# Performance work log

Hardware: AMD Instinct MI355X
Metric: run time of the kernel (lower is better)

Reference implementation:

```python
import jax, jax.numpy as jnp
import numpy as np

N_NODES = 22
K_NEIGHBOR = 4
BN_EPS = 1e-5


def _conv1d(x, w):
    # x: (B, C, L), w: (O, C, 7), stride 1, padding 3
    return jax.lax.conv_general_dilated(x, w, (1,), [(3, 3)],
                                        dimension_numbers=('NCH', 'OIH', 'NCH'))


def _block(x, w, gamma, beta):
    # x: (N, B, C, L) -> conv + per-node BatchNorm (train-mode batch stats,
    # matching the original per-node loop) + ReLU + MaxPool1d(2)
    n, b, c, l = x.shape
    y = _conv1d(x.reshape(n * b, c, l), w)            # (N*B, O, L)
    o, lo = y.shape[1], y.shape[2]
    y = y.reshape(n, b, o, lo)
    mean = y.mean(axis=(1, 3), keepdims=True)
    var = y.var(axis=(1, 3), keepdims=True)
    y = (y - mean) * jax.lax.rsqrt(var + BN_EPS)
    y = y * gamma[None, None, :, None] + beta[None, None, :, None]
    y = jax.nn.relu(y)
    y = y.reshape(n, b, o, lo // 2, 2).max(axis=-1)   # MaxPool1d(2)
    return y


def _adj_matrix(feat, k):
    # feat: (B, N, D). Squared euclidean distances, k nearest (incl. self), row-normalized.
    sq = jnp.sum(feat ** 2, axis=2, keepdims=True)            # (B, N, 1)
    dist = sq + jnp.swapaxes(sq, 1, 2) - 2.0 * jnp.einsum('bnd,bmd->bnm', feat, feat)
    _, idx = jax.lax.top_k(-dist, k)                          # smallest-k indices, (B, N, k)
    adj = jax.nn.one_hot(idx, feat.shape[1], dtype=feat.dtype).sum(axis=2)
    return adj * (1.0 / k)


def setup_inputs() -> dict:
    key = jax.random.key(0)
    ks = jax.random.split(key, 20)
    B, N, T = 256, N_NODES, 2000
    f32 = jnp.float32
    inp = {
        'x': jax.random.normal(ks[0], (B, N, T), f32),
        # conv stack (shared across all electrode nodes)
        'w1': jax.random.normal(ks[1], (4, 1, 7), f32) * 0.2,
        'g1': jnp.ones((4,), f32), 'b1': jnp.zeros((4,), f32),
        'w2': jax.random.normal(ks[2], (8, 4, 7), f32) * 0.1,
        'g2': jnp.ones((8,), f32), 'b2': jnp.zeros((8,), f32),
        'w3': jax.random.normal(ks[3], (16, 8, 7), f32) * 0.1,
        'g3': jnp.ones((16,), f32), 'b3': jnp.zeros((16,), f32),
        # graph convolutions (uniform init like torch module)
        'gw1': jax.random.uniform(ks[4], (16, 32), f32, -1/np.sqrt(32), 1/np.sqrt(32)),
        'gb1': jax.random.uniform(ks[5], (1, 1, 32), f32, -1/np.sqrt(32), 1/np.sqrt(32)),
        'gw2': jax.random.uniform(ks[6], (32, 64), f32, -1/np.sqrt(64), 1/np.sqrt(64)),
        'gb2': jax.random.uniform(ks[7], (1, 1, 64), f32, -1/np.sqrt(64), 1/np.sqrt(64)),
        'gw3': jax.random.uniform(ks[8], (64, 128), f32, -1/np.sqrt(128), 1/np.sqrt(128)),
        'gb3': jax.random.uniform(ks[9], (1, 1, 128), f32, -1/np.sqrt(128), 1/np.sqrt(128)),
        # heads (stored as (in, out))
        'fw1': jax.random.normal(ks[10], (128, 64), f32) * 0.05,
        'fb1': jnp.zeros((64,), f32),
        'fw2': jax.random.normal(ks[11], (64, 4), f32) * 0.05,
        'fb2': jnp.zeros((4,), f32),
    }
    return inp


def reference(x, w1, g1, b1, w2, g2, b2, w3, g3, b3,
              gw1, gb1, gw2, gb2, gw3, gb3, fw1, fb1, fw2, fb2):
    B, N, T = x.shape
    # --- MultiChannelConv (vectorized over electrode nodes) ---
    h = jnp.transpose(x, (1, 0, 2))[:, :, None, :]   # (N, B, 1, T)
    h = _block(h, w1, g1, b1)                        # (N, B, 4, T/2)
    h = _block(h, w2, g2, b2)                        # (N, B, 8, T/4)
    h = _block(h, w3, g3, b3)                        # (N, B, 16, T/8)
    feat = h.mean(axis=-1)                           # AdaptiveAvgPool1d(1) -> (N, B, 16)
    feat = jnp.transpose(feat, (1, 0, 2))            # (B, N, 16)
    # --- adjacency from top-k nearest neighbors ---
    adj = _adj_matrix(feat, K_NEIGHBOR)              # (B, N, N)
    # --- graph convolutions ---
    x1 = jax.nn.relu(jnp.einsum('bnm,bmf->bnf', adj, feat @ gw1) + gb1)
    x2 = jax.nn.relu(jnp.einsum('bnm,bmf->bnf', adj, x1 @ gw2) + gb2)
    x3 = jax.nn.relu(jnp.einsum('bnm,bmf->bnf', adj, x2 @ gw3) + gb3)
    # mean over nodes, then MLP head
    pooled = x3.mean(axis=1)                         # (B, 128)
    out = (pooled @ fw1 + fb1) @ fw2 + fb2           # (B, nclass)
    return out
```

## Files before the change

kernel.cpp:

```cpp
#include <hip/hip_runtime.h>

#define BSZ 256
#define NND 22
#define BN_EPS 1e-5f

template<int CIN, int COUT, int R, int SROW>
__device__ __forceinline__ void conv_coreR(
    const float (*s_in)[SROW], const float* s_w, int tid, float y[COUT][R]) {
#pragma unroll
  for (int o = 0; o < COUT; o++)
#pragma unroll
    for (int r = 0; r < R; r++) y[o][r] = 0.f;
#pragma unroll 1
  for (int c = 0; c < CIN; c++) {
    float xr[R + 6];
    if constexpr (R == 4) {
      const float4* xp = (const float4*)&s_in[c][4 * tid];
      float4 xa = xp[0], xb = xp[1];
      float2 xc = *(const float2*)&s_in[c][4 * tid + 8];
      xr[0] = xa.x; xr[1] = xa.y; xr[2] = xa.z; xr[3] = xa.w;
      xr[4] = xb.x; xr[5] = xb.y; xr[6] = xb.z; xr[7] = xb.w;
      xr[8] = xc.x; xr[9] = xc.y;
    } else {
      const float2* xp = (const float2*)&s_in[c][2 * tid];
      float2 x0 = xp[0], x1 = xp[1], x2 = xp[2], x3 = xp[3];
      xr[0] = x0.x; xr[1] = x0.y; xr[2] = x1.x; xr[3] = x1.y;
      xr[4] = x2.x; xr[5] = x2.y; xr[6] = x3.x; xr[7] = x3.y;
    }
#pragma unroll
    for (int k = 0; k < 7; k++) {
      const float4* wp = (const float4*)&s_w[(c * 7 + k) * COUT];
#pragma unroll
      for (int o4 = 0; o4 < COUT / 4; o4++) {
        float4 wv = wp[o4];
#pragma unroll
        for (int r = 0; r < R; r++) {
          y[4 * o4 + 0][r] += wv.x * xr[r + k];
          y[4 * o4 + 1][r] += wv.y * xr[r + k];
          y[4 * o4 + 2][r] += wv.z * xr[r + k];
          y[4 * o4 + 3][r] += wv.w * xr[r + k];
        }
      }
    }
  }
}

template<int CIN, int COUT, int NTH>
__device__ __forceinline__ void stage_weights(const float* __restrict__ w,
                                              float* s_w, int tid) {
  for (int i = tid; i < CIN * 7 * COUT; i += NTH) {
    int c = i / (7 * COUT), k = (i / COUT) % 7, o = i % COUT;
    s_w[i] = w[(o * CIN + c) * 7 + k];
  }
}

__global__ __launch_bounds__(256) void prep_weights(
    const float* __restrict__ w2, const float* __restrict__ w3,
    float* __restrict__ w2t, float* __restrict__ w3t) {
  int tid = threadIdx.x;
  if (tid < 224) {
    int c = tid / 56, k = (tid / 8) % 7, o = tid & 7;
    w2t[tid] = w2[(o * 4 + c) * 7 + k];
  }
  for (int i = tid; i < 896; i += 256) {
    int c = i / 112, k = (i / 16) % 7, o = i & 15;
    w3t[i] = w3[(o * 8 + c) * 7 + k];
  }
}

template<int CIN, int COUT, int LIN, int NTH, int NT, int R>
__global__ __launch_bounds__(NTH) void conv_statsR(
    const float* __restrict__ in, long sn, long sb, long sc,
    const float* __restrict__ w, float* __restrict__ part) {
  const int TILE = R * NTH;
  const int SROW = TILE + 8;
  __shared__ alignas(16) float s_in[CIN][SROW];
  __shared__ alignas(16) float s_w[CIN * 7 * COUT];
  __shared__ float s_red[2][NTH / 64][COUT];
  int tid = threadIdx.x, n = blockIdx.z, b = blockIdx.y;
  int t0 = blockIdx.x * TILE;
  const float* base = in + (long)n * sn + (long)b * sb;
  stage_weights<CIN, COUT, NTH>(w, s_w, tid);
  for (int c = 0; c < CIN; c++)
    for (int i = tid; i < TILE + 6; i += NTH) {
      int l = t0 + i - 3;
      s_in[c][i] = (l >= 0 && l < LIN) ? base[(long)c * sc + l] : 0.f;
    }
  __syncthreads();
  float y[COUT][R];
  conv_coreR<CIN, COUT, R, SROW>(s_in, s_w, tid, y);
  bool valid = (t0 + R * tid) < LIN;
  int lane = tid & 63, wv = tid >> 6;
#pragma unroll
  for (int o = 0; o < COUT; o++) {
    float s = 0.f, q = 0.f;
    if (valid) {
#pragma unroll
      for (int r = 0; r < R; r++) { s += y[o][r]; q += y[o][r] * y[o][r]; }
    }
#pragma unroll
    for (int off = 32; off > 0; off >>= 1) {
      s += __shfl_down(s, off, 64);
      q += __shfl_down(q, off, 64);
    }
    if (lane == 0) { s_red[0][wv][o] = s; s_red[1][wv][o] = q; }
  }
  __syncthreads();
  if (tid < COUT) {
    float s = 0.f, q = 0.f;
#pragma unroll
    for (int g = 0; g < NTH / 64; g++) { s += s_red[0][g][tid]; q += s_red[1][g][tid]; }
    long slot = ((long)n * NT + blockIdx.x) * BSZ + b;
    part[slot * (2 * COUT) + tid] = s;
    part[slot * (2 * COUT) + COUT + tid] = q;
  }
}

template<int C, int NSLOT, int LIN>
__global__ __launch_bounds__(256) void stats_reduce(
    const float* __restrict__ part,
    const float* __restrict__ gamma, const float* __restrict__ beta,
    float* __restrict__ scs) {
  const int V = 2 * C;
  const int GRP = 256 / V;
  int n = blockIdx.x, tid = threadIdx.x;
  int j = tid % V, g = tid / V;
  const float* p = part + (long)n * NSLOT * V;
  float s = 0.f;
  for (int sl = g; sl < NSLOT; sl += GRP) s += p[(long)sl * V + j];
  __shared__ float red[V][GRP];
  __shared__ float tot[V];
  red[j][g] = s;
  __syncthreads();
  if (tid < V) {
    float t = 0.f;
#pragma unroll
    for (int gg = 0; gg < GRP; gg++) t += red[tid][gg];
    tot[tid] = t;
  }
  __syncthreads();
  if (tid < C) {
    float cnt = (float)BSZ * (float)LIN;
    float m = tot[tid] / cnt;
    float var = tot[C + tid] / cnt - m * m;
    float istd = 1.0f / sqrtf(var + BN_EPS);
    float scl = gamma[tid] * istd;
    scs[n * 64 + tid] = scl;
    scs[n * 64 + 32 + tid] = beta[tid] - m * scl;
  }
}

__global__ __launch_bounds__(256) void fused1(
    const float* __restrict__ x,
    const float* __restrict__ w1,
    const float* __restrict__ scs1,
    const float* __restrict__ w2t,
    float* __restrict__ y2p,
    float* __restrict__ p2) {
  __shared__ alignas(16) float s_x[2016];
  __shared__ alignas(16) float s_h1[4][1008];
  __shared__ float s_sc[4], s_sh[4];
  __shared__ float s_red[2][4][8];
  int tid = threadIdx.x, n = blockIdx.z, b = blockIdx.y;
  const float* xb = x + (long)b * (NND * 2000) + (long)n * 2000;
  if (tid < 4) { s_sc[tid] = scs1[n * 64 + tid]; s_sh[tid] = scs1[n * 64 + 32 + tid]; }
  for (int i = tid; i < 500; i += 256)
    *(float4*)&s_x[4 * i + 4] = *(const float4*)&xb[4 * i];
  if (tid == 0) {
    *(float4*)&s_x[0] = make_float4(0.f, 0.f, 0.f, 0.f);
    *(float4*)&s_x[2004] = make_float4(0.f, 0.f, 0.f, 0.f);
  }
  __syncthreads();
  if (tid < 250) {
    float xr[16];
    const float4* xp = (const float4*)&s_x[8 * tid];
#pragma unroll
    for (int v = 0; v < 4; v++) {
      float4 t = xp[v];
      xr[4 * v + 0] = t.x; xr[4 * v + 1] = t.y;
      xr[4 * v + 2] = t.z; xr[4 * v + 3] = t.w;
    }
    float y[4][8];
#pragma unroll
    for (int o = 0; o < 4; o++)
#pragma unroll
      for (int r = 0; r < 8; r++) y[o][r] = 0.f;
#pragma unroll
    for (int k = 0; k < 7; k++) {
      float w0 = w1[0 * 7 + k], w1v = w1[1 * 7 + k];
      float w2v = w1[2 * 7 + k], w3v = w1[3 * 7 + k];
#pragma unroll
      for (int r = 0; r < 8; r++) {
        y[0][r] += w0 * xr[r + k + 1];
        y[1][r] += w1v * xr[r + k + 1];
        y[2][r] += w2v * xr[r + k + 1];
        y[3][r] += w3v * xr[r + k + 1];
      }
    }
#pragma unroll
    for (int o = 0; o < 4; o++) {
      float a0 = y[o][0] * s_sc[o] + s_sh[o], a1 = y[o][1] * s_sc[o] + s_sh[o];
      float a2 = y[o][2] * s_sc[o] + s_sh[o], a3 = y[o][3] * s_sc[o] + s_sh[o];
      float a4 = y[o][4] * s_sc[o] + s_sh[o], a5 = y[o][5] * s_sc[o] + s_sh[o];
      float a6 = y[o][6] * s_sc[o] + s_sh[o], a7 = y[o][7] * s_sc[o] + s_sh[o];
      float4 v;
      v.x = fmaxf(fmaxf(a0, a1), 0.f);
      v.y = fmaxf(fmaxf(a2, a3), 0.f);
      v.z = fmaxf(fmaxf(a4, a5), 0.f);
      v.w = fmaxf(fmaxf(a6, a7), 0.f);
      *(float4*)&s_h1[o][4 * tid + 4] = v;
    }
  }
  if (tid < 4) {
    *(float4*)&s_h1[tid][0] = make_float4(0.f, 0.f, 0.f, 0.f);
    *(float4*)&s_h1[tid][1004] = make_float4(0.f, 0.f, 0.f, 0.f);
  }
  __syncthreads();
  float y2[8][4];
#pragma unroll
  for (int o = 0; o < 8; o++)
#pragma unroll
    for (int r = 0; r < 4; r++) y2[o][r] = 0.f;
  if (tid < 250) {
#pragma unroll 1
    for (int c = 0; c < 4; c++) {
      float xr[12];
      const float4* xp = (const float4*)&s_h1[c][4 * tid];
#pragma unroll
      for (int v = 0; v < 3; v++) {
        float4 t = xp[v];
        xr[4 * v + 0] = t.x; xr[4 * v + 1] = t.y;
        xr[4 * v + 2] = t.z; xr[4 * v + 3] = t.w;
      }
#pragma unroll
      for (int k = 0; k < 7; k++) {
        float4 w0 = *(const float4*)&w2t[(c * 7 + k) * 8];
        float4 w1v = *(const float4*)&w2t[(c * 7 + k) * 8 + 4];
#pragma unroll
        for (int r = 0; r < 4; r++) {
          float xv = xr[r + k + 1];
          y2[0][r] += w0.x * xv;
          y2[1][r] += w0.y * xv;
          y2[2][r] += w0.z * xv;
          y2[3][r] += w0.w * xv;
          y2[4][r] += w1v.x * xv;
          y2[5][r] += w1v.y * xv;
          y2[6][r] += w1v.z * xv;
          y2[7][r] += w1v.w * xv;
        }
      }
    }
    long yb = ((long)n * BSZ + b) * 4000 + 2 * tid;
#pragma unroll
    for (int o = 0; o < 8; o++) {
      float2 v;
      v.x = fmaxf(y2[o][0], y2[o][1]);
      v.y = fmaxf(y2[o][2], y2[o][3]);
      *(float2*)&y2p[yb + o * 500] = v;
    }
  }
  int lane = tid & 63, wv = tid >> 6;
#pragma unroll
  for (int o = 0; o < 8; o++) {
    float s = y2[o][0] + y2[o][1] + y2[o][2] + y2[o][3];
    float q = y2[o][0] * y2[o][0] + y2[o][1] * y2[o][1] +
              y2[o][2] * y2[o][2] + y2[o][3] * y2[o][3];
#pragma unroll
    for (int off = 32; off > 0; off >>= 1) {
      s += __shfl_down(s, off, 64);
      q += __shfl_down(q, off, 64);
    }
    if (lane == 0) { s_red[0][wv][o] = s; s_red[1][wv][o] = q; }
  }
  __syncthreads();
  if (tid < 8) {
    float s = 0.f, q = 0.f;
#pragma unroll
    for (int g = 0; g < 4; g++) { s += s_red[0][g][tid]; q += s_red[1][g][tid]; }
    long slot = (long)n * BSZ + b;
    p2[slot * 16 + tid] = s;
    p2[slot * 16 + 8 + tid] = q;
  }
}

__global__ __launch_bounds__(256) void fused2(
    const float* __restrict__ y2p,
    const float* __restrict__ scs2,
    const float* __restrict__ w3t,
    float* __restrict__ y3p,
    float* __restrict__ p3) {
  __shared__ alignas(16) float s_h2[8][512];
  __shared__ float s_sc[8], s_sh[8];
  __shared__ float s_red[2][4][8];
  int tid = threadIdx.x, n = blockIdx.z, b = blockIdx.y;
  if (tid < 8) { s_sc[tid] = scs2[n * 64 + tid]; s_sh[tid] = scs2[n * 64 + 32 + tid]; }
  __syncthreads();
  const float* yb2 = y2p + ((long)n * BSZ + b) * 4000;
  for (int i = tid; i < 1000; i += 256) {
    int ch = i / 125, j4 = i % 125;
    float4 v = *(const float4*)&yb2[ch * 500 + 4 * j4];
    float sc = s_sc[ch], sh = s_sh[ch];
    v.x = fmaxf(v.x * sc + sh, 0.f);
    v.y = fmaxf(v.y * sc + sh, 0.f);
    v.z = fmaxf(v.z * sc + sh, 0.f);
    v.w = fmaxf(v.w * sc + sh, 0.f);
    *(float4*)&s_h2[ch][4 * j4 + 4] = v;
  }
  if (tid < 8) {
    *(float4*)&s_h2[tid][0] = make_float4(0.f, 0.f, 0.f, 0.f);
    *(float4*)&s_h2[tid][504] = make_float4(0.f, 0.f, 0.f, 0.f);
  }
  __syncthreads();
  int og = __builtin_amdgcn_readfirstlane(tid >> 7);
  int pt = tid & 127;
  bool valid = pt < 125;
  float y3[8][4];
#pragma unroll
  for (int o = 0; o < 8; o++)
#pragma unroll
    for (int r = 0; r < 4; r++) y3[o][r] = 0.f;
  if (valid) {
#pragma unroll 1
    for (int c = 0; c < 8; c++) {
      float xr[12];
      const float4* xp = (const float4*)&s_h2[c][4 * pt];
#pragma unroll
      for (int v = 0; v < 3; v++) {
        float4 t = xp[v];
        xr[4 * v + 0] = t.x; xr[4 * v + 1] = t.y;
        xr[4 * v + 2] = t.z; xr[4 * v + 3] = t.w;
      }
#pragma unroll
      for (int k = 0; k < 7; k++) {
        float4 w0 = *(const float4*)&w3t[(c * 7 + k) * 16 + og * 8];
        float4 w1v = *(const float4*)&w3t[(c * 7 + k) * 16 + og * 8 + 4];
#pragma unroll
        for (int r = 0; r < 4; r++) {
          float xv = xr[r + k + 1];
          y3[0][r] += w0.x * xv;
          y3[1][r] += w0.y * xv;
          y3[2][r] += w0.z * xv;
          y3[3][r] += w0.w * xv;
          y3[4][r] += w1v.x * xv;
          y3[5][r] += w1v.y * xv;
          y3[6][r] += w1v.z * xv;
          y3[7][r] += w1v.w * xv;
        }
      }
    }
    long yb = (((long)n * BSZ + b) * 16 + og * 8) * 250 + 2 * pt;
#pragma unroll
    for (int o = 0; o < 8; o++) {
      float2 v;
      v.x = fmaxf(y3[o][0], y3[o][1]);
      v.y = fmaxf(y3[o][2], y3[o][3]);
      *(float2*)&y3p[yb + o * 250] = v;
    }
  }
  int lane = tid & 63, wv = tid >> 6;
#pragma unroll
  for (int o = 0; o < 8; o++) {
    float s = y3[o][0] + y3[o][1] + y3[o][2] + y3[o][3];
    float q = y3[o][0] * y3[o][0] + y3[o][1] * y3[o][1] +
              y3[o][2] * y3[o][2] + y3[o][3] * y3[o][3];
#pragma unroll
    for (int off = 32; off > 0; off >>= 1) {
      s += __shfl_down(s, off, 64);
      q += __shfl_down(q, off, 64);
    }
    if (lane == 0) { s_red[0][wv][o] = s; s_red[1][wv][o] = q; }
  }
  __syncthreads();
  if (tid < 16) {
    int og2 = tid >> 3, o = tid & 7;
    float s = s_red[0][2 * og2][o] + s_red[0][2 * og2 + 1][o];
    float q = s_red[1][2 * og2][o] + s_red[1][2 * og2 + 1][o];
    long slot = (long)n * BSZ + b;
    p3[slot * 32 + tid] = s;
    p3[slot * 32 + 16 + tid] = q;
  }
}

__global__ __launch_bounds__(256) void feat_apply(
    const float* __restrict__ y3p,
    const float* __restrict__ scs3,
    float* __restrict__ feat) {
  int tid = threadIdx.x, n = blockIdx.z, b = blockIdx.y;
  int ch = tid >> 4, s = tid & 15;
  const float* yb = y3p + (((long)n * BSZ + b) * 16 + ch) * 250;
  float sc = scs3[n * 64 + ch], sh = scs3[n * 64 + 32 + ch];
  float acc = 0.f;
  for (int j = s; j < 125; j += 16) {
    float2 v = *(const float2*)&yb[2 * j];
    acc += fmaxf(v.x * sc + sh, 0.f) + fmaxf(v.y * sc + sh, 0.f);
  }
#pragma unroll
  for (int off = 8; off > 0; off >>= 1) acc += __shfl_down(acc, off, 16);
  if (s == 0) feat[((long)b * NND + n) * 16 + ch] = acc * (1.0f / 250.f);
}

__global__ __launch_bounds__(256) void graph_head(
    const float* __restrict__ feat,
    const float* __restrict__ gw1, const float* __restrict__ gb1,
    const float* __restrict__ gw2, const float* __restrict__ gb2,
    const float* __restrict__ gw3, const float* __restrict__ gb3,
    const float* __restrict__ fw1, const float* __restrict__ fb1,
    const float* __restrict__ fw2, const float* __restrict__ fb2,
    float* __restrict__ out) {
  int b = blockIdx.x, tid = threadIdx.x;
  __shared__ float s_feat[NND][16];
  __shared__ float s_sq[NND];
  __shared__ float s_dist[NND][NND];
  __shared__ float s_adj[NND][NND];
  __shared__ float s_x[NND][128];
  __shared__ float s_t[NND][128];
  __shared__ float s_pool[128];
  __shared__ float s_h[64];
  for (int i = tid; i < NND * 16; i += 256) s_feat[i >> 4][i & 15] = feat[b * NND * 16 + i];
  __syncthreads();
  if (tid < NND) {
    float s = 0.f;
    for (int c = 0; c < 16; c++) s += s_feat[tid][c] * s_feat[tid][c];
    s_sq[tid] = s;
  }
  __syncthreads();
  for (int i = tid; i < NND * NND; i += 256) {
    int nn = i / NND, m = i % NND;
    float d = 0.f;
    for (int c = 0; c < 16; c++) d += s_feat[nn][c] * s_feat[m][c];
    s_dist[nn][m] = s_sq[nn] + s_sq[m] - 2.f * d;
    s_adj[nn][m] = 0.f;
  }
  __syncthreads();
  if (tid < NND) {
    unsigned used = 0;
    for (int j = 0; j < 4; j++) {
      float best = 3.4e38f; int bi = 0;
      for (int m = 0; m < NND; m++)
        if (!((used >> m) & 1u) && s_dist[tid][m] < best) { best = s_dist[tid][m]; bi = m; }
      used |= 1u << bi;
      s_adj[tid][bi] = 0.25f;
    }
  }
  __syncthreads();
  for (int i = tid; i < NND * 32; i += 256) {
    int nn = i / 32, f = i % 32;
    float a = 0.f;
    for (int c = 0; c < 16; c++) a += s_feat[nn][c] * gw1[c * 32 + f];
    s_t[nn][f] = a;
  }
  __syncthreads();
  for (int i = tid; i < NND * 32; i += 256) {
    int nn = i / 32, f = i % 32;
    float a = gb1[f];
    for (int m = 0; m < NND; m++) a += s_adj[nn][m] * s_t[m][f];
    s_x[nn][f] = fmaxf(a, 0.f);
  }
  __syncthreads();
  for (int i = tid; i < NND * 64; i += 256) {
    int nn = i / 64, f = i % 64;
    float a = 0.f;
    for (int c = 0; c < 32; c++) a += s_x[nn][c] * gw2[c * 64 + f];
    s_t[nn][f] = a;
  }
  __syncthreads();
  for (int i = tid; i < NND * 64; i += 256) {
    int nn = i / 64, f = i % 64;
    float a = gb2[f];
    for (int m = 0; m < NND; m++) a += s_adj[nn][m] * s_t[m][f];
    s_x[nn][f] = fmaxf(a, 0.f);
  }
  __syncthreads();
  for (int i = tid; i < NND * 128; i += 256) {
    int nn = i / 128, f = i % 128;
    float a = 0.f;
    for (int c = 0; c < 64; c++) a += s_x[nn][c] * gw3[c * 128 + f];
    s_t[nn][f] = a;
  }
  __syncthreads();
  for (int i = tid; i < NND * 128; i += 256) {
    int nn = i / 128, f = i % 128;
    float a = gb3[f];
    for (int m = 0; m < NND; m++) a += s_adj[nn][m] * s_t[m][f];
    s_x[nn][f] = fmaxf(a, 0.f);
  }
  __syncthreads();
  if (tid < 128) {
    float a = 0.f;
    for (int m = 0; m < NND; m++) a += s_x[m][tid];
    s_pool[tid] = a * (1.0f / (float)NND);
  }
  __syncthreads();
  if (tid < 64) {
    float a = fb1[tid];
    for (int c = 0; c < 128; c++) a += s_pool[c] * fw1[c * 64 + tid];
    s_h[tid] = a;
  }
  __syncthreads();
  if (tid < 4) {
    float a = fb2[tid];
    for (int c = 0; c < 64; c++) a += s_h[c] * fw2[c * 4 + tid];
    out[b * 4 + tid] = a;
  }
}

extern "C" void kernel_launch(void* const* d_in, const int* in_sizes, int n_in,
                              void* d_out, int out_size, void* d_ws, size_t ws_size,
                              hipStream_t stream) {
  (void)in_sizes; (void)n_in; (void)out_size; (void)ws_size;
  const float* x   = (const float*)d_in[0];
  const float* w1  = (const float*)d_in[1];
  const float* g1  = (const float*)d_in[2];
  const float* b1  = (const float*)d_in[3];
  const float* w2  = (const float*)d_in[4];
  const float* g2  = (const float*)d_in[5];
  const float* b2  = (const float*)d_in[6];
  const float* w3  = (const float*)d_in[7];
  const float* g3  = (const float*)d_in[8];
  const float* b3  = (const float*)d_in[9];
  const float* gw1 = (const float*)d_in[10];
  const float* gb1 = (const float*)d_in[11];
  const float* gw2 = (const float*)d_in[12];
  const float* gb2 = (const float*)d_in[13];
  const float* gw3 = (const float*)d_in[14];
  const float* gb3 = (const float*)d_in[15];
  const float* fw1 = (const float*)d_in[16];
  const float* fb1 = (const float*)d_in[17];
  const float* fw2 = (const float*)d_in[18];
  const float* fb2 = (const float*)d_in[19];

  float* ws = (float*)d_ws;
  const long Y2 = (long)NND * BSZ * 8 * 500;
  const long Y3 = (long)NND * BSZ * 16 * 250;
  float* y2p  = ws;
  float* y3p  = y2p + Y2;
  float* feat = y3p + Y3;
  float* scs1 = feat + (long)BSZ * NND * 16;
  float* scs2 = scs1 + NND * 64;
  float* scs3 = scs2 + NND * 64;
  float* p1   = scs3 + NND * 64;
  float* p2   = p1 + (long)NND * 512 * 8;
  float* p3   = p2 + (long)NND * 256 * 16;
  float* w2t  = p3 + (long)NND * 256 * 32;
  float* w3t  = w2t + 224;

  prep_weights<<<dim3(1), dim3(256), 0, stream>>>(w2, w3, w2t, w3t);
  conv_statsR<1, 4, 2000, 256, 2, 4><<<dim3(2, BSZ, NND), dim3(256), 0, stream>>>(
      x, 2000, (long)NND * 2000, 0, w1, p1);
  stats_reduce<4, 512, 2000><<<dim3(NND), dim3(256), 0, stream>>>(p1, g1, b1, scs1);
  fused1<<<dim3(1, BSZ, NND), dim3(256), 0, stream>>>(x, w1, scs1, w2t, y2p, p2);
  stats_reduce<8, 256, 1000><<<dim3(NND), dim3(256), 0, stream>>>(p2, g2, b2, scs2);
  fused2<<<dim3(1, BSZ, NND), dim3(256), 0, stream>>>(y2p, scs2, w3t, y3p, p3);
  stats_reduce<16, 256, 500><<<dim3(NND), dim3(256), 0, stream>>>(p3, g3, b3, scs3);
  feat_apply<<<dim3(1, BSZ, NND), dim3(256), 0, stream>>>(y3p, scs3, feat);
  graph_head<<<dim3(BSZ), dim3(256), 0, stream>>>(
      feat, gw1, gb1, gw2, gb2, gw3, gb3, fw1, fb1, fw2, fb2, (float*)d_out);
}
```

Before: 222.7 us.

## Fuse feature pooling into graph head, merge weight prep, prefetch conv inputs

Removes the separate prep_weights and feat_apply launches: weight transposition moves into the first stats_reduce, and the per-node BN+ReLU+mean pooling moves into graph_head, which loops over all 22 nodes per batch block. Global loads in fused1/fused2 are issued up front, and channel rows from shared memory are prefetched one iteration ahead using an extra padded row. This cuts launch overhead and the feat round-trip. In exchange, the large y3p read is now done by only 256 blocks instead of 5632, which reduces memory-level parallelism.

```diff
diff --git a/kernel.cpp b/kernel.cpp
--- a/kernel.cpp
+++ b/kernel.cpp
@@ -51,20 +51,6 @@
   for (int i = tid; i < CIN * 7 * COUT; i += NTH) {
     int c = i / (7 * COUT), k = (i / COUT) % 7, o = i % COUT;
     s_w[i] = w[(o * CIN + c) * 7 + k];
-  }
-}
-
-__global__ __launch_bounds__(256) void prep_weights(
-    const float* __restrict__ w2, const float* __restrict__ w3,
-    float* __restrict__ w2t, float* __restrict__ w3t) {
-  int tid = threadIdx.x;
-  if (tid < 224) {
-    int c = tid / 56, k = (tid / 8) % 7, o = tid & 7;
-    w2t[tid] = w2[(o * 4 + c) * 7 + k];
-  }
-  for (int i = tid; i < 896; i += 256) {
-    int c = i / 112, k = (i / 16) % 7, o = i & 15;
-    w3t[i] = w3[(o * 8 + c) * 7 + k];
   }
 }
 
@@ -120,7 +106,9 @@
 __global__ __launch_bounds__(256) void stats_reduce(
     const float* __restrict__ part,
     const float* __restrict__ gamma, const float* __restrict__ beta,
-    float* __restrict__ scs) {
+    float* __restrict__ scs,
+    const float* __restrict__ w2, const float* __restrict__ w3,
+    float* __restrict__ w2t, float* __restrict__ w3t) {
   const int V = 2 * C;
   const int GRP = 256 / V;
   int n = blockIdx.x, tid = threadIdx.x;
@@ -148,6 +136,16 @@
     scs[n * 64 + tid] = scl;
     scs[n * 64 + 32 + tid] = beta[tid] - m * scl;
   }
+  if (w2t != nullptr && blockIdx.x == 0) {
+    if (tid < 224) {
+      int c = tid / 56, k = (tid / 8) % 7, o = tid & 7;
+      w2t[tid] = w2[(o * 4 + c) * 7 + k];
+    }
+    for (int i = tid; i < 896; i += 256) {
+      int c = i / 112, k = (i / 16) % 7, o = i & 15;
+      w3t[i] = w3[(o * 8 + c) * 7 + k];
+    }
+  }
 }
 
 __global__ __launch_bounds__(256) void fused1(
@@ -158,14 +156,20 @@
     float* __restrict__ y2p,
     float* __restrict__ p2) {
   __shared__ alignas(16) float s_x[2016];
-  __shared__ alignas(16) float s_h1[4][1008];
+  __shared__ alignas(16) float s_h1[5][1008];
   __shared__ float s_sc[4], s_sh[4];
   __shared__ float s_red[2][4][8];
   int tid = threadIdx.x, n = blockIdx.z, b = blockIdx.y;
   const float* xb = x + (long)b * (NND * 2000) + (long)n * 2000;
   if (tid < 4) { s_sc[tid] = scs1[n * 64 + tid]; s_sh[tid] = scs1[n * 64 + 32 + tid]; }
-  for (int i = tid; i < 500; i += 256)
-    *(float4*)&s_x[4 * i + 4] = *(const float4*)&xb[4 * i];
+  {
+    float4 a0 = *(const float4*)&xb[4 * tid];
+    float4 a1;
+    bool m1 = tid + 256 < 500;
+    if (m1) a1 = *(const float4*)&xb[4 * (tid + 256)];
+    *(float4*)&s_x[4 * tid + 4] = a0;
+    if (m1) *(float4*)&s_x[4 * (tid + 256) + 4] = a1;
+  }
   if (tid == 0) {
     *(float4*)&s_x[0] = make_float4(0.f, 0.f, 0.f, 0.f);
     *(float4*)&s_x[2004] = make_float4(0.f, 0.f, 0.f, 0.f);
@@ -222,16 +226,17 @@
 #pragma unroll
     for (int r = 0; r < 4; r++) y2[o][r] = 0.f;
   if (tid < 250) {
+    const float4* xp0 = (const float4*)&s_h1[0][4 * tid];
+    float4 n0 = xp0[0], n1 = xp0[1], n2 = xp0[2];
 #pragma unroll 1
     for (int c = 0; c < 4; c++) {
+      float4 c0 = n0, c1 = n1, c2 = n2;
+      const float4* xpn = (const float4*)&s_h1[c + 1][4 * tid];
+      n0 = xpn[0]; n1 = xpn[1]; n2 = xpn[2];
       float xr[12];
-      const float4* xp = (const float4*)&s_h1[c][4 * tid];
-#pragma unroll
-      for (int v = 0; v < 3; v++) {
-        float4 t = xp[v];
-        xr[4 * v + 0] = t.x; xr[4 * v + 1] = t.y;
-        xr[4 * v + 2] = t.z; xr[4 * v + 3] = t.w;
-      }
+      xr[0] = c0.x; xr[1] = c0.y; xr[2] = c0.z; xr[3] = c0.w;
+      xr[4] = c1.x; xr[5] = c1.y; xr[6] = c1.z; xr[7] = c1.w;
+      xr[8] = c2.x; xr[9] = c2.y; xr[10] = c2.z; xr[11] = c2.w;
 #pragma unroll
       for (int k = 0; k < 7; k++) {
         float4 w0 = *(const float4*)&w2t[(c * 7 + k) * 8];
@@ -289,22 +294,44 @@
     const float* __restrict__ w3t,
     float* __restrict__ y3p,
     float* __restrict__ p3) {
-  __shared__ alignas(16) float s_h2[8][512];
+  __shared__ alignas(16) float s_h2[9][512];
   __shared__ float s_sc[8], s_sh[8];
   __shared__ float s_red[2][4][8];
   int tid = threadIdx.x, n = blockIdx.z, b = blockIdx.y;
   if (tid < 8) { s_sc[tid] = scs2[n * 64 + tid]; s_sh[tid] = scs2[n * 64 + 32 + tid]; }
   __syncthreads();
   const float* yb2 = y2p + ((long)n * BSZ + b) * 4000;
-  for (int i = tid; i < 1000; i += 256) {
-    int ch = i / 125, j4 = i % 125;
-    float4 v = *(const float4*)&yb2[ch * 500 + 4 * j4];
-    float sc = s_sc[ch], sh = s_sh[ch];
-    v.x = fmaxf(v.x * sc + sh, 0.f);
-    v.y = fmaxf(v.y * sc + sh, 0.f);
-    v.z = fmaxf(v.z * sc + sh, 0.f);
-    v.w = fmaxf(v.w * sc + sh, 0.f);
-    *(float4*)&s_h2[ch][4 * j4 + 4] = v;
+  {
+    int i0 = tid, i1 = tid + 256, i2 = tid + 512, i3 = tid + 768;
+    int c0 = i0 / 125, j0 = i0 % 125;
+    int c1 = i1 / 125, j1 = i1 % 125;
+    int c2 = i2 / 125, j2 = i2 % 125;
+    int c3 = i3 / 125, j3 = i3 % 125;
+    bool m3 = i3 < 1000;
+    float4 a0 = *(const float4*)&yb2[c0 * 500 + 4 * j0];
+    float4 a1 = *(const float4*)&yb2[c1 * 500 + 4 * j1];
+    float4 a2 = *(const float4*)&yb2[c2 * 500 + 4 * j2];
+    float4 a3;
+    if (m3) a3 = *(const float4*)&yb2[c3 * 500 + 4 * j3];
+    float sc, sh;
+    sc = s_sc[c0]; sh = s_sh[c0];
+    a0.x = fmaxf(a0.x * sc + sh, 0.f); a0.y = fmaxf(a0.y * sc + sh, 0.f);
+    a0.z = fmaxf(a0.z * sc + sh, 0.f); a0.w = fmaxf(a0.w * sc + sh, 0.f);
+    *(float4*)&s_h2[c0][4 * j0 + 4] = a0;
+    sc = s_sc[c1]; sh = s_sh[c1];
+    a1.x = fmaxf(a1.x * sc + sh, 0.f); a1.y = fmaxf(a1.y * sc + sh, 0.f);
+    a1.z = fmaxf(a1.z * sc + sh, 0.f); a1.w = fmaxf(a1.w * sc + sh, 0.f);
+    *(float4*)&s_h2[c1][4 * j1 + 4] = a1;
+    sc = s_sc[c2]; sh = s_sh[c2];
+    a2.x = fmaxf(a2.x * sc + sh, 0.f); a2.y = fmaxf(a2.y * sc + sh, 0.f);
+    a2.z = fmaxf(a2.z * sc + sh, 0.f); a2.w = fmaxf(a2.w * sc + sh, 0.f);
+    *(float4*)&s_h2[c2][4 * j2 + 4] = a2;
+    if (m3) {
+      sc = s_sc[c3]; sh = s_sh[c3];
+      a3.x = fmaxf(a3.x * sc + sh, 0.f); a3.y = fmaxf(a3.y * sc + sh, 0.f);
+      a3.z = fmaxf(a3.z * sc + sh, 0.f); a3.w = fmaxf(a3.w * sc + sh, 0.f);
+      *(float4*)&s_h2[c3][4 * j3 + 4] = a3;
+    }
   }
   if (tid < 8) {
     *(float4*)&s_h2[tid][0] = make_float4(0.f, 0.f, 0.f, 0.f);
@@ -320,16 +347,17 @@
 #pragma unroll
     for (int r = 0; r < 4; r++) y3[o][r] = 0.f;
   if (valid) {
+    const float4* xp0 = (const float4*)&s_h2[0][4 * pt];
+    float4 n0 = xp0[0], n1 = xp0[1], n2 = xp0[2];
 #pragma unroll 1
     for (int c = 0; c < 8; c++) {
+      float4 c0 = n0, c1 = n1, c2 = n2;
+      const float4* xpn = (const float4*)&s_h2[c + 1][4 * pt];
+      n0 = xpn[0]; n1 = xpn[1]; n2 = xpn[2];
       float xr[12];
-      const float4* xp = (const float4*)&s_h2[c][4 * pt];
-#pragma unroll
-      for (int v = 0; v < 3; v++) {
-        float4 t = xp[v];
-        xr[4 * v + 0] = t.x; xr[4 * v + 1] = t.y;
-        xr[4 * v + 2] = t.z; xr[4 * v + 3] = t.w;
-      }
+      xr[0] = c0.x; xr[1] = c0.y; xr[2] = c0.z; xr[3] = c0.w;
+      xr[4] = c1.x; xr[5] = c1.y; xr[6] = c1.z; xr[7] = c1.w;
+      xr[8] = c2.x; xr[9] = c2.y; xr[10] = c2.z; xr[11] = c2.w;
 #pragma unroll
       for (int k = 0; k < 7; k++) {
         float4 w0 = *(const float4*)&w3t[(c * 7 + k) * 16 + og * 8];
@@ -381,26 +409,9 @@
   }
 }
 
-__global__ __launch_bounds__(256) void feat_apply(
+__global__ __launch_bounds__(256) void graph_head(
     const float* __restrict__ y3p,
     const float* __restrict__ scs3,
-    float* __restrict__ feat) {
-  int tid = threadIdx.x, n = blockIdx.z, b = blockIdx.y;
-  int ch = tid >> 4, s = tid & 15;
-  const float* yb = y3p + (((long)n * BSZ + b) * 16 + ch) * 250;
-  float sc = scs3[n * 64 + ch], sh = scs3[n * 64 + 32 + ch];
-  float acc = 0.f;
-  for (int j = s; j < 125; j += 16) {
-    float2 v = *(const float2*)&yb[2 * j];
-    acc += fmaxf(v.x * sc + sh, 0.f) + fmaxf(v.y * sc + sh, 0.f);
-  }
-#pragma unroll
-  for (int off = 8; off > 0; off >>= 1) acc += __shfl_down(acc, off, 16);
-  if (s == 0) feat[((long)b * NND + n) * 16 + ch] = acc * (1.0f / 250.f);
-}
-
-__global__ __launch_bounds__(256) void graph_head(
-    const float* __restrict__ feat,
     const float* __restrict__ gw1, const float* __restrict__ gb1,
     const float* __restrict__ gw2, const float* __restrict__ gb2,
     const float* __restrict__ gw3, const float* __restrict__ gb3,
@@ -416,7 +427,21 @@
   __shared__ float s_t[NND][128];
   __shared__ float s_pool[128];
   __shared__ float s_h[64];
-  for (int i = tid; i < NND * 16; i += 256) s_feat[i >> 4][i & 15] = feat[b * NND * 16 + i];
+  {
+    int g = tid >> 4, s = tid & 15;
+    for (int nn = 0; nn < NND; nn++) {
+      const float* yb = y3p + (((long)nn * BSZ + b) * 16 + g) * 250;
+      float sc = scs3[nn * 64 + g], sh = scs3[nn * 64 + 32 + g];
+      float acc = 0.f;
+      for (int j = s; j < 125; j += 16) {
+        float2 v = *(const float2*)&yb[2 * j];
+        acc += fmaxf(v.x * sc + sh, 0.f) + fmaxf(v.y * sc + sh, 0.f);
+      }
+#pragma unroll
+      for (int off = 8; off > 0; off >>= 1) acc += __shfl_down(acc, off, 16);
+      if (s == 0) s_feat[nn][g] = acc * (1.0f / 250.f);
+    }
+  }
   __syncthreads();
   if (tid < NND) {
     float s = 0.f;
@@ -534,8 +559,7 @@
   const long Y3 = (long)NND * BSZ * 16 * 250;
   float* y2p  = ws;
   float* y3p  = y2p + Y2;
-  float* feat = y3p + Y3;
-  float* scs1 = feat + (long)BSZ * NND * 16;
+  float* scs1 = y3p + Y3;
   float* scs2 = scs1 + NND * 64;
   float* scs3 = scs2 + NND * 64;
   float* p1   = scs3 + NND * 64;
@@ -544,15 +568,16 @@
   float* w2t  = p3 + (long)NND * 256 * 32;
   float* w3t  = w2t + 224;
 
-  prep_weights<<<dim3(1), dim3(256), 0, stream>>>(w2, w3, w2t, w3t);
   conv_statsR<1, 4, 2000, 256, 2, 4><<<dim3(2, BSZ, NND), dim3(256), 0, stream>>>(
       x, 2000, (long)NND * 2000, 0, w1, p1);
-  stats_reduce<4, 512, 2000><<<dim3(NND), dim3(256), 0, stream>>>(p1, g1, b1, scs1);
+  stats_reduce<4, 512, 2000><<<dim3(NND), dim3(256), 0, stream>>>(
+      p1, g1, b1, scs1, w2, w3, w2t, w3t);
   fused1<<<dim3(1, BSZ, NND), dim3(256), 0, stream>>>(x, w1, scs1, w2t, y2p, p2);
-  stats_reduce<8, 256, 1000><<<dim3(NND), dim3(256), 0, stream>>>(p2, g2, b2, scs2);
+  stats_reduce<8, 256, 1000><<<dim3(NND), dim3(256), 0, stream>>>(
+      p2, g2, b2, scs2, nullptr, nullptr, nullptr, nullptr);
   fused2<<<dim3(1, BSZ, NND), dim3(256), 0, stream>>>(y2p, scs2, w3t, y3p, p3);
-  stats_reduce<16, 256, 500><<<dim3(NND), dim3(256), 0, stream>>>(p3, g3, b3, scs3);
-  feat_apply<<<dim3(1, BSZ, NND), dim3(256), 0, stream>>>(y3p, scs3, feat);
+  stats_reduce<16, 256, 500><<<dim3(NND), dim3(256), 0, stream>>>(
+      p3, g3, b3, scs3, nullptr, nullptr, nullptr, nullptr);
   graph_head<<<dim3(BSZ), dim3(256), 0, stream>>>(
-      feat, gw1, gb1, gw2, gb2, gw3, gb3, fw1, fb1, fw2, fb2, (float*)d_out);
-}
+      y3p, scs3, gw1, gb1, gw2, gb2, gw3, gb3, fw1, fb1, fw2, fb2, (float*)d_out);
+}
```

Result: slower. 255.1 us (+14.6%).
